# Performance work log

Hardware: AMD Instinct MI355X
Metric: run time of the kernel (lower is better)

The kernel has to match this reference:

```python
import jax, jax.numpy as jnp
import numpy as np

B, C_IN, N, E, C_OUT = 1, 128, 50000, 800000, 128
NEG_SLOPE = 0.3


def setup_inputs() -> dict:
    key = jax.random.key(0)
    k1, k2, k3, k4, k5 = jax.random.split(key, 5)
    in_features = jax.random.normal(k1, (B, C_IN, N), dtype=jnp.float32)
    weight = jax.random.normal(k2, (C_OUT, 2 * C_IN), dtype=jnp.float32) / np.sqrt(2 * C_IN)
    bias = jax.random.normal(k3, (C_OUT,), dtype=jnp.float32) * 0.01
    reduce_index = jax.random.randint(k4, (E,), 0, N, dtype=jnp.int64)
    gather_index = jax.random.randint(k5, (E,), 0, N, dtype=jnp.int64)
    return {"in_features": in_features, "weight": weight, "bias": bias,
            "reduce_index": reduce_index, "gather_index": gather_index}


def reference(in_features, weight, bias, reduce_index, gather_index):
    n_vertices = in_features.shape[-1]
    # gather endpoint features: [B, C, E]
    vertices = in_features[..., reduce_index]
    neighbors = in_features[..., gather_index]
    # concat [x_i, x_j - x_i] -> [B, 2C, E]
    concat = jnp.concatenate([vertices, neighbors - vertices], axis=1)
    # 1x1 Conv1d == per-edge matmul: [B, O, E]
    f_e = jnp.einsum('oc,bce->boe', weight, concat) + bias[None, :, None]
    # scatter-mean over reduce_index (include_self=False: empty segments stay 0)
    f_e_efirst = jnp.moveaxis(f_e, -1, 0)                      # [E, B, O]
    sums = jax.ops.segment_sum(f_e_efirst, reduce_index, num_segments=n_vertices)  # [N,B,O]
    counts = jax.ops.segment_sum(jnp.ones((reduce_index.shape[0],), dtype=f_e.dtype),
                                 reduce_index, num_segments=n_vertices)            # [N]
    mean = sums / jnp.maximum(counts, 1.0)[:, None, None]
    out = jnp.moveaxis(mean, 0, -1)                            # [B, O, N]
    # LeakyReLU(0.3)
    return jnp.where(out >= 0, out, NEG_SLOPE * out)
```

## Files before the change

### kernel.cpp

```cpp
#include <hip/hip_runtime.h>
#include <stddef.h>

#define CCH 128
#define CAP 64
#define FILL_CS 4096

typedef unsigned int  uint;
typedef unsigned short ushort;
typedef short bf16x8 __attribute__((ext_vector_type(8)));
typedef float f32x4  __attribute__((ext_vector_type(4)));

__device__ __forceinline__ ushort f2bf(float f) {
    uint b = __float_as_uint(f);
    b += 0x7FFFu + ((b >> 16) & 1u);
    return (ushort)(b >> 16);
}
__device__ __forceinline__ float bflo(uint u) { return __uint_as_float(u << 16); }
__device__ __forceinline__ float bfhi(uint u) { return __uint_as_float(u & 0xFFFF0000u); }

__global__ void prep_zero(const float* __restrict__ w, ushort* __restrict__ wstb,
                          int* __restrict__ zero_buf, int NZ) {
    int i = blockIdx.x * 256 + threadIdx.x;
    if (i < CCH * 256) {
        int c = i & 255;
        float v = w[i];
        if (c < 128) v -= w[i + 128];
        wstb[i] = f2bf(v);
    }
    for (int n = i; n < NZ; n += gridDim.x * 256) zero_buf[n] = 0;
}

__global__ __launch_bounds__(256) void transpose_fill(
        const float* __restrict__ x, ushort* __restrict__ xtb,
        const int* __restrict__ ridx, const int* __restrict__ gidx,
        int* __restrict__ counts, int* __restrict__ bucket,
        int N, int E, int psz, int T, int F) {
    __shared__ float tile[CCH][33];
    int b = blockIdx.x;
    int mtf = (T < F) ? T : F;
    int twice = 2 * mtf;
    bool is_t; int sub;
    if (b < twice) { is_t = !(b & 1); sub = b >> 1; }
    else           { is_t = (T > F);  sub = (b - twice) + mtf; }
    int tid = threadIdx.x;

    if (is_t) {
        int n0 = sub * 32;
        {
            int tx = tid & 31, r = tid >> 5;
            int n = n0 + tx;
            #pragma unroll
            for (int k = 0; k < 16; ++k) {
                int c = k * 8 + r;
                tile[c][tx] = (n < N) ? x[(size_t)c * N + n] : 0.f;
            }
        }
        __syncthreads();
        #pragma unroll
        for (int p = 0; p < 2; ++p) {
            int nn = p * 16 + (tid >> 4);
            int c8 = (tid & 15) * 8;
            if (n0 + nn < N) {
                ushort u[8];
                #pragma unroll
                for (int j = 0; j < 8; ++j) u[j] = f2bf(tile[c8 + j][nn]);
                uint4 v;
                v.x = (uint)u[0] | ((uint)u[1] << 16);
                v.y = (uint)u[2] | ((uint)u[3] << 16);
                v.z = (uint)u[4] | ((uint)u[5] << 16);
                v.w = (uint)u[6] | ((uint)u[7] << 16);
                *(uint4*)(xtb + (size_t)(n0 + nn) * CCH + c8) = v;
            }
        }
    } else {
        int part  = sub & 7;
        int chunk = sub >> 3;
        int e0 = chunk * FILL_CS;
        int e1 = e0 + FILL_CS; if (e1 > E) e1 = E;
        for (int base = e0; base < e1; base += 1024) {
            int rr[4], gg[4];
            bool act[4];
            #pragma unroll
            for (int q = 0; q < 4; ++q) {
                int e = base + q * 256 + tid;
                bool in = (e < e1);
                int ec = in ? e : e0;
                rr[q] = ridx[ec];
                gg[q] = gidx[ec];
                act[q] = in && (rr[q] / psz == part);
            }
            #pragma unroll
            for (int q = 0; q < 4; ++q) {
                if (act[q]) {
                    int p = atomicAdd(&counts[rr[q]], 1);
                    if (p < CAP) bucket[rr[q] * CAP + p] = gg[q];
                }
            }
        }
    }
}

__global__ __launch_bounds__(256) void gather_mean(
        const uint2* __restrict__ xtb,
        const int*   __restrict__ counts,
        const int*   __restrict__ bucket,
        ushort*      __restrict__ gmb,
        int N) {
    int wave = threadIdx.x >> 6;
    int l = threadIdx.x & 63;
    int lq = l & 31;
    int half = l >> 5;
    #pragma unroll
    for (int i = 0; i < 2; ++i) {
        int n = blockIdx.x * 8 + wave * 2 + i;
        if (n >= N) return;
        int deg = __builtin_amdgcn_readfirstlane(counts[n]);
        int dg  = (deg < CAP) ? deg : CAP;
        const int* row = bucket + n * CAP;
        float4 acc = make_float4(0.f, 0.f, 0.f, 0.f);
        int k = 0;
        for (; k + 16 <= dg; k += 16) {
            uint2 u[8];
            #pragma unroll
            for (int q = 0; q < 8; ++q) {
                int g = row[k + 2 * q + half];
                u[q] = xtb[(size_t)g * 32 + lq];
            }
            #pragma unroll
            for (int q = 0; q < 8; ++q) {
                acc.x += bflo(u[q].x); acc.y += bfhi(u[q].x);
                acc.z += bflo(u[q].y); acc.w += bfhi(u[q].y);
            }
        }
        for (; k + 8 <= dg; k += 8) {
            uint2 u[4];
            #pragma unroll
            for (int q = 0; q < 4; ++q) {
                int g = row[k + 2 * q + half];
                u[q] = xtb[(size_t)g * 32 + lq];
            }
            #pragma unroll
            for (int q = 0; q < 4; ++q) {
                acc.x += bflo(u[q].x); acc.y += bfhi(u[q].x);
                acc.z += bflo(u[q].y); acc.w += bfhi(u[q].y);
            }
        }
        for (; k + 2 <= dg; k += 2) {
            int g = row[k + half];
            uint2 u = xtb[(size_t)g * 32 + lq];
            acc.x += bflo(u.x); acc.y += bfhi(u.x);
            acc.z += bflo(u.y); acc.w += bfhi(u.y);
        }
        if (k < dg && half == 0) {
            int g = row[k];
            uint2 u = xtb[(size_t)g * 32 + lq];
            acc.x += bflo(u.x); acc.y += bfhi(u.x);
            acc.z += bflo(u.y); acc.w += bfhi(u.y);
        }
        acc.x += __shfl_xor(acc.x, 32);
        acc.y += __shfl_xor(acc.y, 32);
        acc.z += __shfl_xor(acc.z, 32);
        acc.w += __shfl_xor(acc.w, 32);
        float inv = (deg > 0) ? 1.f / (float)deg : 0.f;
        if (half == 0) {
            ushort4 r;
            r.x = f2bf(acc.x * inv);
            r.y = f2bf(acc.y * inv);
            r.z = f2bf(acc.z * inv);
            r.w = f2bf(acc.w * inv);
            *(ushort4*)(gmb + (size_t)n * CCH + lq * 4) = r;
        }
    }
}

__global__ __launch_bounds__(256) void gemm_mfma(
        const ushort* __restrict__ wstb,
        const ushort* __restrict__ xtb,
        const ushort* __restrict__ gmb,
        const int*    __restrict__ counts,
        const float*  __restrict__ bias,
        float* __restrict__ out,
        int N) {
    int t = threadIdx.x;
    int wv = t >> 6;
    int l  = t & 63;
    int l15 = l & 15;
    int lk  = l >> 4;
    int n = blockIdx.x * 64 + wv * 16 + l15;
    int nc = (n < N) ? n : (N - 1);

    f32x4 acc[8];
    #pragma unroll
    for (int mf = 0; mf < 8; ++mf) acc[mf] = (f32x4){0.f, 0.f, 0.f, 0.f};

    const ushort* brow_x = xtb + (size_t)nc * CCH + lk * 8;
    const ushort* brow_g = gmb + (size_t)nc * CCH + lk * 8;
    const ushort* arow   = wstb + (size_t)l15 * 256 + lk * 8;

    #pragma unroll
    for (int ks = 0; ks < 8; ++ks) {
        const ushort* bp = (ks < 4) ? (brow_x + ks * 32) : (brow_g + (ks - 4) * 32);
        bf16x8 b = *(const bf16x8*)bp;
        #pragma unroll
        for (int mf = 0; mf < 8; ++mf) {
            bf16x8 a = *(const bf16x8*)(arow + (size_t)mf * 16 * 256 + ks * 32);
            acc[mf] = __builtin_amdgcn_mfma_f32_16x16x32_bf16(a, b, acc[mf], 0, 0, 0);
        }
    }

    if (n < N) {
        float m = (counts[n] > 0) ? 1.f : 0.f;
        #pragma unroll
        for (int mf = 0; mf < 8; ++mf) {
            #pragma unroll
            for (int r = 0; r < 4; ++r) {
                int o = mf * 16 + lk * 4 + r;
                float v = (acc[mf][r] + bias[o]) * m;
                v = (v >= 0.f) ? v : 0.3f * v;
                out[(size_t)o * N + n] = v;
            }
        }
    }
}

extern "C" void kernel_launch(void* const* d_in, const int* in_sizes, int n_in,
                              void* d_out, int out_size, void* d_ws, size_t ws_size,
                              hipStream_t stream) {
    const float* x      = (const float*)d_in[0];
    const float* weight = (const float*)d_in[1];
    const float* bias   = (const float*)d_in[2];
    const int*   ridx   = (const int*)d_in[3];
    const int*   gidx   = (const int*)d_in[4];
    float* out = (float*)d_out;

    int N = in_sizes[0] / CCH;
    int E = in_sizes[3];

    char* ws = (char*)d_ws;
    size_t xtb_bytes = (((size_t)N * CCH * sizeof(ushort)) + 63) & ~(size_t)63;
    size_t n_bytes   = (((size_t)N * sizeof(int)) + 63) & ~(size_t)63;
    size_t bkt_bytes = (((size_t)N * CAP * sizeof(int)) + 63) & ~(size_t)63;
    size_t w_bytes   = (((size_t)CCH * 256 * sizeof(ushort)) + 63) & ~(size_t)63;

    size_t o = 0;
    ushort* xtb   = (ushort*)(ws + o); o += xtb_bytes;
    int*    counts= (int*)   (ws + o); o += n_bytes;
    int*    bucket= (int*)   (ws + o); o += bkt_bytes;
    ushort* wstb  = (ushort*)(ws + o); o += w_bytes;
    ushort* gmb   = (ushort*)(ws + o);

    int psz     = (N + 7) / 8;
    int nchunks = (E + FILL_CS - 1) / FILL_CS;
    int T = (N + 31) / 32;
    int F = nchunks * 8;

    prep_zero<<<128, 256, 0, stream>>>(weight, wstb, counts, N);

    transpose_fill<<<T + F, 256, 0, stream>>>(x, xtb, ridx, gidx,
                                              counts, bucket, N, E, psz, T, F);

    gather_mean<<<(N + 7) / 8, 256, 0, stream>>>(
        (const uint2*)xtb, counts, bucket, gmb, N);

    gemm_mfma<<<(N + 63) / 64, 256, 0, stream>>>(
        wstb, xtb, gmb, counts, bias, out, N);
}
```

Baseline: 121.2 us.

## Fuse neighbor gather-mean into MFMA GEMM kernel, dropping intermediate buffer

Merges the separate gather_mean and gemm_mfma kernels into one. Each lane now gathers and averages its node's neighbor rows directly into registers in the layout of the MFMA B fragment, then runs the GEMM. This removes one launch and the bf16 intermediate written to and read back from global memory. In exchange each lane handles one node serially, with loop length set by the max degree across 16 lanes, so more registers are used and the gather has less memory-level parallelism than the wave-per-node scheme. Occupancy and latency hiding may suffer.

```diff
diff --git a/kernel.cpp b/kernel.cpp
--- a/kernel.cpp
+++ b/kernel.cpp
@@ -100,84 +100,11 @@
     }
 }
 
-__global__ __launch_bounds__(256) void gather_mean(
-        const uint2* __restrict__ xtb,
-        const int*   __restrict__ counts,
-        const int*   __restrict__ bucket,
-        ushort*      __restrict__ gmb,
-        int N) {
-    int wave = threadIdx.x >> 6;
-    int l = threadIdx.x & 63;
-    int lq = l & 31;
-    int half = l >> 5;
-    #pragma unroll
-    for (int i = 0; i < 2; ++i) {
-        int n = blockIdx.x * 8 + wave * 2 + i;
-        if (n >= N) return;
-        int deg = __builtin_amdgcn_readfirstlane(counts[n]);
-        int dg  = (deg < CAP) ? deg : CAP;
-        const int* row = bucket + n * CAP;
-        float4 acc = make_float4(0.f, 0.f, 0.f, 0.f);
-        int k = 0;
-        for (; k + 16 <= dg; k += 16) {
-            uint2 u[8];
-            #pragma unroll
-            for (int q = 0; q < 8; ++q) {
-                int g = row[k + 2 * q + half];
-                u[q] = xtb[(size_t)g * 32 + lq];
-            }
-            #pragma unroll
-            for (int q = 0; q < 8; ++q) {
-                acc.x += bflo(u[q].x); acc.y += bfhi(u[q].x);
-                acc.z += bflo(u[q].y); acc.w += bfhi(u[q].y);
-            }
-        }
-        for (; k + 8 <= dg; k += 8) {
-            uint2 u[4];
-            #pragma unroll
-            for (int q = 0; q < 4; ++q) {
-                int g = row[k + 2 * q + half];
-                u[q] = xtb[(size_t)g * 32 + lq];
-            }
-            #pragma unroll
-            for (int q = 0; q < 4; ++q) {
-                acc.x += bflo(u[q].x); acc.y += bfhi(u[q].x);
-                acc.z += bflo(u[q].y); acc.w += bfhi(u[q].y);
-            }
-        }
-        for (; k + 2 <= dg; k += 2) {
-            int g = row[k + half];
-            uint2 u = xtb[(size_t)g * 32 + lq];
-            acc.x += bflo(u.x); acc.y += bfhi(u.x);
-            acc.z += bflo(u.y); acc.w += bfhi(u.y);
-        }
-        if (k < dg && half == 0) {
-            int g = row[k];
-            uint2 u = xtb[(size_t)g * 32 + lq];
-            acc.x += bflo(u.x); acc.y += bfhi(u.x);
-            acc.z += bflo(u.y); acc.w += bfhi(u.y);
-        }
-        acc.x += __shfl_xor(acc.x, 32);
-        acc.y += __shfl_xor(acc.y, 32);
-        acc.z += __shfl_xor(acc.z, 32);
-        acc.w += __shfl_xor(acc.w, 32);
-        float inv = (deg > 0) ? 1.f / (float)deg : 0.f;
-        if (half == 0) {
-            ushort4 r;
-            r.x = f2bf(acc.x * inv);
-            r.y = f2bf(acc.y * inv);
-            r.z = f2bf(acc.z * inv);
-            r.w = f2bf(acc.w * inv);
-            *(ushort4*)(gmb + (size_t)n * CCH + lq * 4) = r;
-        }
-    }
-}
-
-__global__ __launch_bounds__(256) void gemm_mfma(
+__global__ __launch_bounds__(256) void gather_gemm(
+        const ushort* __restrict__ xtb,
+        const int*    __restrict__ counts,
+        const int*    __restrict__ bucket,
         const ushort* __restrict__ wstb,
-        const ushort* __restrict__ xtb,
-        const ushort* __restrict__ gmb,
-        const int*    __restrict__ counts,
         const float*  __restrict__ bias,
         float* __restrict__ out,
         int N) {
@@ -189,18 +116,72 @@
     int n = blockIdx.x * 64 + wv * 16 + l15;
     int nc = (n < N) ? n : (N - 1);
 
+    int deg_full = counts[nc];
+    int deg = (deg_full < CAP) ? deg_full : CAP;
+    if (n >= N) deg = 0;
+    int dmax = deg;
+    #pragma unroll
+    for (int off = 1; off < 16; off <<= 1) {
+        int o2 = __shfl_xor(dmax, off);
+        dmax = (o2 > dmax) ? o2 : dmax;
+    }
+
+    const int* brow = bucket + (size_t)nc * CAP;
+    float ga[4][8];
+    #pragma unroll
+    for (int q = 0; q < 4; ++q)
+        #pragma unroll
+        for (int e = 0; e < 8; ++e) ga[q][e] = 0.f;
+
+    for (int k = 0; k < dmax; k += 2) {
+        bool a0 = (k < deg), a1 = (k + 1 < deg);
+        int g0 = nc, g1 = nc;
+        if (a0) g0 = brow[k];
+        if (a1) g1 = brow[k + 1];
+        const ushort* r0 = xtb + (size_t)g0 * CCH + lk * 8;
+        const ushort* r1 = xtb + (size_t)g1 * CCH + lk * 8;
+        uint4 u0[4], u1[4];
+        #pragma unroll
+        for (int q = 0; q < 4; ++q) {
+            u0[q] = *(const uint4*)(r0 + q * 32);
+            u1[q] = *(const uint4*)(r1 + q * 32);
+        }
+        #pragma unroll
+        for (int q = 0; q < 4; ++q) {
+            if (a0) {
+                ga[q][0] += bflo(u0[q].x); ga[q][1] += bfhi(u0[q].x);
+                ga[q][2] += bflo(u0[q].y); ga[q][3] += bfhi(u0[q].y);
+                ga[q][4] += bflo(u0[q].z); ga[q][5] += bfhi(u0[q].z);
+                ga[q][6] += bflo(u0[q].w); ga[q][7] += bfhi(u0[q].w);
+            }
+            if (a1) {
+                ga[q][0] += bflo(u1[q].x); ga[q][1] += bfhi(u1[q].x);
+                ga[q][2] += bflo(u1[q].y); ga[q][3] += bfhi(u1[q].y);
+                ga[q][4] += bflo(u1[q].z); ga[q][5] += bfhi(u1[q].z);
+                ga[q][6] += bflo(u1[q].w); ga[q][7] += bfhi(u1[q].w);
+            }
+        }
+    }
+
+    float inv = (deg_full > 0 && n < N) ? 1.f / (float)deg_full : 0.f;
+    const ushort* xrow = xtb + (size_t)nc * CCH + lk * 8;
+    bf16x8 bfrag[8];
+    #pragma unroll
+    for (int q = 0; q < 4; ++q) {
+        bfrag[q] = *(const bf16x8*)(xrow + q * 32);
+        bf16x8 v;
+        #pragma unroll
+        for (int e = 0; e < 8; ++e) v[e] = (short)f2bf(ga[q][e] * inv);
+        bfrag[4 + q] = v;
+    }
+
     f32x4 acc[8];
     #pragma unroll
     for (int mf = 0; mf < 8; ++mf) acc[mf] = (f32x4){0.f, 0.f, 0.f, 0.f};
-
-    const ushort* brow_x = xtb + (size_t)nc * CCH + lk * 8;
-    const ushort* brow_g = gmb + (size_t)nc * CCH + lk * 8;
-    const ushort* arow   = wstb + (size_t)l15 * 256 + lk * 8;
-
+    const ushort* arow = wstb + (size_t)l15 * 256 + lk * 8;
     #pragma unroll
     for (int ks = 0; ks < 8; ++ks) {
-        const ushort* bp = (ks < 4) ? (brow_x + ks * 32) : (brow_g + (ks - 4) * 32);
-        bf16x8 b = *(const bf16x8*)bp;
+        bf16x8 b = bfrag[ks];
         #pragma unroll
         for (int mf = 0; mf < 8; ++mf) {
             bf16x8 a = *(const bf16x8*)(arow + (size_t)mf * 16 * 256 + ks * 32);
@@ -209,7 +190,7 @@
     }
 
     if (n < N) {
-        float m = (counts[n] > 0) ? 1.f : 0.f;
+        float m = (deg_full > 0) ? 1.f : 0.f;
         #pragma unroll
         for (int mf = 0; mf < 8; ++mf) {
             #pragma unroll
@@ -247,7 +228,6 @@
     int*    counts= (int*)   (ws + o); o += n_bytes;
     int*    bucket= (int*)   (ws + o); o += bkt_bytes;
     ushort* wstb  = (ushort*)(ws + o); o += w_bytes;
-    ushort* gmb   = (ushort*)(ws + o);
 
     int psz     = (N + 7) / 8;
     int nchunks = (E + FILL_CS - 1) / FILL_CS;
@@ -259,9 +239,6 @@
     transpose_fill<<<T + F, 256, 0, stream>>>(x, xtb, ridx, gidx,
                                               counts, bucket, N, E, psz, T, F);
 
-    gather_mean<<<(N + 7) / 8, 256, 0, stream>>>(
-        (const uint2*)xtb, counts, bucket, gmb, N);
-
-    gemm_mfma<<<(N + 63) / 64, 256, 0, stream>>>(
-        wstb, xtb, gmb, counts, bias, out, N);
-}
+    gather_gemm<<<(N + 63) / 64, 256, 0, stream>>>(
+        xtb, counts, bucket, wstb, bias, out, N);
+}
```

Result: slower. 139.5 us (+15.1%).

## Fuse neighbor-mean gather into MFMA GEMM via swizzled LDS staging

Applied to the files above, without the earlier changes.

Merges the gather_mean and gemm_mfma kernels into one kernel. Each block of 64 vertices first computes neighbor means into a swizzled LDS tile, syncs, then runs the MFMA GEMM reading the mean half of the B operand from LDS instead of a global intermediate. This removes the global write and re-read of the bf16 mean buffer and one kernel launch. In exchange, each block now does 16 vertices per wave serially and uses 16 KB of LDS, which lowers the number of vertices in flight per block during the latency-bound gather phase and may reduce occupancy.

```diff
diff --git a/kernel.cpp b/kernel.cpp
--- a/kernel.cpp
+++ b/kernel.cpp
@@ -100,23 +100,30 @@
     }
 }
 
-__global__ __launch_bounds__(256) void gather_mean(
-        const uint2* __restrict__ xtb,
-        const int*   __restrict__ counts,
-        const int*   __restrict__ bucket,
-        ushort*      __restrict__ gmb,
+__global__ __launch_bounds__(256) void gather_gemm_lds(
+        const uint2*  __restrict__ xtb2,
+        const ushort* __restrict__ xtb,
+        const int*    __restrict__ counts,
+        const int*    __restrict__ bucket,
+        const ushort* __restrict__ wstb,
+        const float*  __restrict__ bias,
+        float* __restrict__ out,
         int N) {
-    int wave = threadIdx.x >> 6;
-    int l = threadIdx.x & 63;
+    __shared__ ushort gt[64 * 128];
+    int t = threadIdx.x;
+    int wv = t >> 6;
+    int l  = t & 63;
     int lq = l & 31;
     int half = l >> 5;
-    #pragma unroll
-    for (int i = 0; i < 2; ++i) {
-        int n = blockIdx.x * 8 + wave * 2 + i;
-        if (n >= N) return;
-        int deg = __builtin_amdgcn_readfirstlane(counts[n]);
-        int dg  = (deg < CAP) ? deg : CAP;
-        const int* row = bucket + n * CAP;
+    int n0 = blockIdx.x * 64;
+
+    for (int i = 0; i < 16; ++i) {
+        int v = wv * 16 + i;
+        int n = n0 + v;
+        int deg = 0;
+        if (n < N) deg = __builtin_amdgcn_readfirstlane(counts[n]);
+        int dg = (deg < CAP) ? deg : CAP;
+        const int* row = bucket + (size_t)((n < N) ? n : 0) * CAP;
         float4 acc = make_float4(0.f, 0.f, 0.f, 0.f);
         int k = 0;
         for (; k + 16 <= dg; k += 16) {
@@ -124,7 +131,7 @@
             #pragma unroll
             for (int q = 0; q < 8; ++q) {
                 int g = row[k + 2 * q + half];
-                u[q] = xtb[(size_t)g * 32 + lq];
+                u[q] = xtb2[(size_t)g * 32 + lq];
             }
             #pragma unroll
             for (int q = 0; q < 8; ++q) {
@@ -137,7 +144,7 @@
             #pragma unroll
             for (int q = 0; q < 4; ++q) {
                 int g = row[k + 2 * q + half];
-                u[q] = xtb[(size_t)g * 32 + lq];
+                u[q] = xtb2[(size_t)g * 32 + lq];
             }
             #pragma unroll
             for (int q = 0; q < 4; ++q) {
@@ -147,13 +154,13 @@
         }
         for (; k + 2 <= dg; k += 2) {
             int g = row[k + half];
-            uint2 u = xtb[(size_t)g * 32 + lq];
+            uint2 u = xtb2[(size_t)g * 32 + lq];
             acc.x += bflo(u.x); acc.y += bfhi(u.x);
             acc.z += bflo(u.y); acc.w += bfhi(u.y);
         }
         if (k < dg && half == 0) {
             int g = row[k];
-            uint2 u = xtb[(size_t)g * 32 + lq];
+            uint2 u = xtb2[(size_t)g * 32 + lq];
             acc.x += bflo(u.x); acc.y += bfhi(u.x);
             acc.z += bflo(u.y); acc.w += bfhi(u.y);
         }
@@ -168,39 +175,34 @@
             r.y = f2bf(acc.y * inv);
             r.z = f2bf(acc.z * inv);
             r.w = f2bf(acc.w * inv);
-            *(ushort4*)(gmb + (size_t)n * CCH + lq * 4) = r;
-        }
-    }
-}
-
-__global__ __launch_bounds__(256) void gemm_mfma(
-        const ushort* __restrict__ wstb,
-        const ushort* __restrict__ xtb,
-        const ushort* __restrict__ gmb,
-        const int*    __restrict__ counts,
-        const float*  __restrict__ bias,
-        float* __restrict__ out,
-        int N) {
-    int t = threadIdx.x;
-    int wv = t >> 6;
-    int l  = t & 63;
+            int uoff = (lq * 4) ^ ((v & 15) << 3);
+            *(ushort4*)&gt[v * 128 + uoff] = r;
+        }
+    }
+    __syncthreads();
+
     int l15 = l & 15;
     int lk  = l >> 4;
-    int n = blockIdx.x * 64 + wv * 16 + l15;
+    int v = wv * 16 + l15;
+    int n = n0 + v;
     int nc = (n < N) ? n : (N - 1);
+
+    bf16x8 bfr[8];
+    const ushort* brow_x = xtb + (size_t)nc * CCH + lk * 8;
+    #pragma unroll
+    for (int q = 0; q < 4; ++q) {
+        bfr[q] = *(const bf16x8*)(brow_x + q * 32);
+        int uoff = (lk * 8 + q * 32) ^ ((v & 15) << 3);
+        bfr[4 + q] = *(const bf16x8*)&gt[v * 128 + uoff];
+    }
 
     f32x4 acc[8];
     #pragma unroll
     for (int mf = 0; mf < 8; ++mf) acc[mf] = (f32x4){0.f, 0.f, 0.f, 0.f};
-
-    const ushort* brow_x = xtb + (size_t)nc * CCH + lk * 8;
-    const ushort* brow_g = gmb + (size_t)nc * CCH + lk * 8;
-    const ushort* arow   = wstb + (size_t)l15 * 256 + lk * 8;
-
+    const ushort* arow = wstb + (size_t)l15 * 256 + lk * 8;
     #pragma unroll
     for (int ks = 0; ks < 8; ++ks) {
-        const ushort* bp = (ks < 4) ? (brow_x + ks * 32) : (brow_g + (ks - 4) * 32);
-        bf16x8 b = *(const bf16x8*)bp;
+        bf16x8 b = bfr[ks];
         #pragma unroll
         for (int mf = 0; mf < 8; ++mf) {
             bf16x8 a = *(const bf16x8*)(arow + (size_t)mf * 16 * 256 + ks * 32);
@@ -209,15 +211,15 @@
     }
 
     if (n < N) {
-        float m = (counts[n] > 0) ? 1.f : 0.f;
+        float m = (counts[nc] > 0) ? 1.f : 0.f;
         #pragma unroll
         for (int mf = 0; mf < 8; ++mf) {
             #pragma unroll
             for (int r = 0; r < 4; ++r) {
                 int o = mf * 16 + lk * 4 + r;
-                float v = (acc[mf][r] + bias[o]) * m;
-                v = (v >= 0.f) ? v : 0.3f * v;
-                out[(size_t)o * N + n] = v;
+                float vv = (acc[mf][r] + bias[o]) * m;
+                vv = (vv >= 0.f) ? vv : 0.3f * vv;
+                out[(size_t)o * N + n] = vv;
             }
         }
     }
@@ -247,7 +249,6 @@
     int*    counts= (int*)   (ws + o); o += n_bytes;
     int*    bucket= (int*)   (ws + o); o += bkt_bytes;
     ushort* wstb  = (ushort*)(ws + o); o += w_bytes;
-    ushort* gmb   = (ushort*)(ws + o);
 
     int psz     = (N + 7) / 8;
     int nchunks = (E + FILL_CS - 1) / FILL_CS;
@@ -259,9 +260,6 @@
     transpose_fill<<<T + F, 256, 0, stream>>>(x, xtb, ridx, gidx,
                                               counts, bucket, N, E, psz, T, F);
 
-    gather_mean<<<(N + 7) / 8, 256, 0, stream>>>(
-        (const uint2*)xtb, counts, bucket, gmb, N);
-
-    gemm_mfma<<<(N + 63) / 64, 256, 0, stream>>>(
-        wstb, xtb, gmb, counts, bias, out, N);
-}
+    gather_gemm_lds<<<(N + 63) / 64, 256, 0, stream>>>(
+        (const uint2*)xtb, xtb, counts, bucket, wstb, bias, out, N);
+}
```

After: 134.0 us. 1.11x slower.
